# Performance work log

Hardware: AMD Instinct MI355X
Metric: run time of the kernel (lower is better)

## Reference

```python
import jax, jax.numpy as jnp
import numpy as np

B, H = 1024, 256
HP = H // 2  # hyperparams_dim
W_SCALE = 0.08  # kaiming-uniform-like magnitude to keep tanh unsaturated


def setup_inputs() -> dict:
    key = jax.random.key(0)
    ks = jax.random.split(key, 8)
    return {
        "h_0": jax.random.normal(ks[0], (B, 1, H), dtype=jnp.float32),
        "h_t": jax.random.normal(ks[1], (B, 1, H), dtype=jnp.float32),
        "msg": jax.random.normal(ks[2], (B, 1, H), dtype=jnp.float32),
        "c": jax.random.uniform(ks[3], (1,), dtype=jnp.float32),
        "fc1_w": jax.random.normal(ks[4], (HP, H), dtype=jnp.float32) * W_SCALE,
        "fc2_w": jax.random.normal(ks[5], (HP, HP), dtype=jnp.float32) * W_SCALE,
        "fc3_w": jax.random.normal(ks[6], (HP, HP), dtype=jnp.float32) * W_SCALE,
        "fc4_w": jax.random.normal(ks[7], (2 * H * H, HP), dtype=jnp.float32) * W_SCALE,
    }


def reference(h_0, h_t, msg, c, fc1_w, fc2_w, fc3_w, fc4_w):
    # torch code clamps self.c into [0, 1] before use
    cc = jnp.clip(c, 0.0, 1.0)
    h = cc * h_0 + (1.0 - cc) * h_t                     # [B, 1, H]
    x = jnp.tanh(jnp.einsum('bsh,ph->bsp', h, fc1_w))    # [B, 1, HP]
    x = jnp.tanh(jnp.einsum('bsp,qp->bsq', x, fc2_w))    # [B, 1, HP]
    x = jnp.tanh(jnp.einsum('bsq,rq->bsr', x, fc3_w))    # [B, 1, HP]
    f4 = jnp.einsum('bsr,wr->bsw', x, fc4_w)             # [B, 1, 2*H*H]
    g1 = f4[..., : H * H].reshape(-1, H, H)              # [B, H, H]
    g2 = f4[..., H * H :].reshape(-1, H, H)              # [B, H, H]
    # F.linear(msg[i], g) == msg[i] @ g.T, batched over B
    g1_out = jnp.tanh(jnp.einsum('bsh,bkh->bsk', msg, g1))  # [B, 1, H]
    out = jnp.einsum('bsk,bok->bso', g1_out, g2)             # [B, 1, H]
    return out
```

## Files before the change

### kernel.cpp

```cpp
#include <hip/hip_runtime.h>
#include <hip/hip_bf16.h>

#define HDIM 256
#define HPDIM 128

typedef short bf8 __attribute__((ext_vector_type(8)));
typedef float f32x4 __attribute__((ext_vector_type(4)));

__device__ inline unsigned pkbf2(float a, float b) {
  float2 f; f.x = a; f.y = b;
  __hip_bfloat162 h = __float22bfloat162_rn(f);
  unsigned u; __builtin_memcpy(&u, &h, 4); return u;
}
__device__ inline unsigned short bfbits(float v) {
  __hip_bfloat16 h = __float2bfloat16(v);
  unsigned short u; __builtin_memcpy(&u, &h, 2); return u;
}
__device__ inline uint4 pack8u(float4 a, float4 b) {
  uint4 r;
  r.x = pkbf2(a.x, a.y); r.y = pkbf2(a.z, a.w);
  r.z = pkbf2(b.x, b.y); r.w = pkbf2(b.z, b.w);
  return r;
}
__device__ inline float fast_tanh(float x) {
  float t = __expf(2.0f * x);
  return 1.0f - 2.0f * __builtin_amdgcn_rcpf(t + 1.0f);
}

__global__ __launch_bounds__(256) void k_fmt(
    const float* __restrict__ w1, const float* __restrict__ w2,
    const float* __restrict__ w3, const float* __restrict__ msg,
    short* __restrict__ wf, float* __restrict__ msgTT) {
  __shared__ float T[64][257];
  const int t = threadIdx.x;
  if (blockIdx.x < 32) {
    int u = blockIdx.x * 256 + t;
    const float* src; short* dst; int row, c, Kt;
    if (u < 4096)      { src = w1; dst = wf;          Kt = 8; row = u >> 5; c = u & 31; }
    else if (u < 6144) { src = w2; dst = wf + 32768;  Kt = 4; row = (u-4096) >> 4; c = (u-4096) & 15; }
    else               { src = w3; dst = wf + 49152;  Kt = 4; row = (u-6144) >> 4; c = (u-6144) & 15; }
    int ks = c >> 2, q = c & 3, Kd = Kt * 32;
    const float* s = src + row * Kd + ks * 32 + q * 8;
    float4 a = *(const float4*)s, b = *(const float4*)(s + 4);
    int P = row >> 4, r16 = row & 15;
    int outl = ((P * Kt + ks) * 64 + q * 16 + r16);
    *(uint4*)(dst + (size_t)outl * 8) = pack8u(a, b);
  } else {
    const int b0 = (blockIdx.x - 32) * 64;
    #pragma unroll 4
    for (int it = 0; it < 16; ++it) {
      int flat = it * 1024 + t * 4;
      int row = flat >> 8, col = flat & 255;
      float4 v = *(const float4*)(msg + (b0 + row) * HDIM + col);
      T[row][col] = v.x; T[row][col+1] = v.y; T[row][col+2] = v.z; T[row][col+3] = v.w;
    }
    __syncthreads();
    const int bloc = t & 63;
    #pragma unroll 4
    for (int it = 0; it < 16; ++it) {
      int g = it * 4 + (t >> 6);
      float4 v; v.x = T[bloc][g*4]; v.y = T[bloc][g*4+1];
                v.z = T[bloc][g*4+2]; v.w = T[bloc][g*4+3];
      *(float4*)(msgTT + (size_t)g * 4096 + (b0 + bloc) * 4) = v;
    }
  }
}

__global__ __launch_bounds__(256) void k_mlp(
    const float* __restrict__ h0, const float* __restrict__ htv,
    const float* __restrict__ cp, const short* __restrict__ wf,
    short* __restrict__ x3f) {
  __shared__ char hbuf[8192];
  __shared__ char xa[4096];
  __shared__ char xb[4096];
  const int t = threadIdx.x, wave = t >> 6, lane = t & 63;
  const int r16 = lane & 15, quad = lane >> 4;
  const int b0 = blockIdx.x * 16;
  const float cc = fminf(fmaxf(cp[0], 0.f), 1.f);

  #pragma unroll
  for (int it = 0; it < 2; ++it) {
    int flat = it * 2048 + t * 8;
    int row = flat >> 8, col = flat & 255, kb = col >> 3;
    int gi = (b0 + row) * HDIM + col;
    float4 a = *(const float4*)(h0 + gi);
    float4 b = *(const float4*)(htv + gi);
    float4 va, vb;
    va.x = cc*a.x + (1.f-cc)*b.x; va.y = cc*a.y + (1.f-cc)*b.y;
    va.z = cc*a.z + (1.f-cc)*b.z; va.w = cc*a.w + (1.f-cc)*b.w;
    a = *(const float4*)(h0 + gi + 4); b = *(const float4*)(htv + gi + 4);
    vb.x = cc*a.x + (1.f-cc)*b.x; vb.y = cc*a.y + (1.f-cc)*b.y;
    vb.z = cc*a.z + (1.f-cc)*b.z; vb.w = cc*a.w + (1.f-cc)*b.w;
    *(uint4*)(hbuf + row*512 + ((kb ^ (row & 7)) << 4)) = pack8u(va, vb);
  }
  __syncthreads();

  {
    f32x4 acc[2] = {};
    #pragma unroll
    for (int ks = 0; ks < 8; ++ks) {
      bf8 af = *(bf8*)(hbuf + r16*512 + (((ks*4 + quad) ^ (r16 & 7)) << 4));
      #pragma unroll
      for (int nt = 0; nt < 2; ++nt) {
        bf8 bw_ = *(const bf8*)(wf + (size_t)(((wave*2 + nt)*8 + ks)*64 + lane)*8);
        acc[nt] = __builtin_amdgcn_mfma_f32_16x16x32_bf16(af, bw_, acc[nt], 0, 0, 0);
      }
    }
    #pragma unroll
    for (int nt = 0; nt < 2; ++nt)
      #pragma unroll
      for (int i = 0; i < 4; ++i) {
        int row = quad*4 + i, col = wave*32 + nt*16 + r16;
        *(unsigned short*)(xa + row*256 + (((col >> 3) ^ (row & 7)) << 4) + ((col & 7) << 1))
            = bfbits(fast_tanh(acc[nt][i]));
      }
  }
  __syncthreads();
  {
    f32x4 acc[2] = {};
    #pragma unroll
    for (int ks = 0; ks < 4; ++ks) {
      bf8 af = *(bf8*)(xa + r16*256 + (((ks*4 + quad) ^ (r16 & 7)) << 4));
      #pragma unroll
      for (int nt = 0; nt < 2; ++nt) {
        bf8 bw_ = *(const bf8*)(wf + 32768 + (size_t)(((wave*2 + nt)*4 + ks)*64 + lane)*8);
        acc[nt] = __builtin_amdgcn_mfma_f32_16x16x32_bf16(af, bw_, acc[nt], 0, 0, 0);
      }
    }
    #pragma unroll
    for (int nt = 0; nt < 2; ++nt)
      #pragma unroll
      for (int i = 0; i < 4; ++i) {
        int row = quad*4 + i, col = wave*32 + nt*16 + r16;
        *(unsigned short*)(xb + row*256 + (((col >> 3) ^ (row & 7)) << 4) + ((col & 7) << 1))
            = bfbits(fast_tanh(acc[nt][i]));
      }
  }
  __syncthreads();
  {
    f32x4 acc[2] = {};
    #pragma unroll
    for (int ks = 0; ks < 4; ++ks) {
      bf8 af = *(bf8*)(xb + r16*256 + (((ks*4 + quad) ^ (r16 & 7)) << 4));
      #pragma unroll
      for (int nt = 0; nt < 2; ++nt) {
        bf8 bw_ = *(const bf8*)(wf + 49152 + (size_t)(((wave*2 + nt)*4 + ks)*64 + lane)*8);
        acc[nt] = __builtin_amdgcn_mfma_f32_16x16x32_bf16(af, bw_, acc[nt], 0, 0, 0);
      }
    }
    #pragma unroll
    for (int nt = 0; nt < 2; ++nt)
      #pragma unroll
      for (int i = 0; i < 4; ++i) {
        int row = quad*4 + i, col = wave*32 + nt*16 + r16;
        *(unsigned short*)(xa + row*256 + (((col >> 3) ^ (row & 7)) << 4) + ((col & 7) << 1))
            = bfbits(fast_tanh(acc[nt][i]));
      }
  }
  __syncthreads();
  {
    int ks = t >> 6, l = t & 63, q2 = l >> 4, rr = l & 15;
    uint4 d = *(uint4*)(xa + rr*256 + (((ks*4 + q2) ^ (rr & 7)) << 4));
    *(uint4*)(x3f + (size_t)((blockIdx.x*4 + ks)*64 + l)*8) = d;
  }
}

template<int PHASE>
__global__ __launch_bounds__(256, 4) void k_hyper(
    const short* __restrict__ x3f, const float* __restrict__ wTT,
    const float* __restrict__ fc4, float* __restrict__ outp) {
  __shared__ char lds[32768];
  const int kcol = blockIdx.x;
  const int t = threadIdx.x, wave = t >> 6, lane = t & 63;
  const int r16 = lane & 15, quad = lane >> 4;
  const int bw = blockIdx.y * 256 + wave * 64;

  bf8 xf[4][4];
  #pragma unroll
  for (int nt = 0; nt < 4; ++nt)
    #pragma unroll
    for (int ks = 0; ks < 4; ++ks)
      xf[nt][ks] = *(const bf8*)(x3f +
          (size_t)(((blockIdx.y*16 + wave*4 + nt)*4 + ks)*64 + lane)*8);

  const float* src = fc4 + ((size_t)(PHASE ? 65536 : 0) + (size_t)kcol * 256) * HPDIM;
  float gacc[4] = {0.f, 0.f, 0.f, 0.f};

  #pragma unroll 1
  for (int half = 0; half < 2; ++half) {
    #pragma unroll
    for (int it = 0; it < 8; ++it) {
      int flat = it * 2048 + t * 8;
      int row = flat >> 7, kb = t & 15;
      float4 a = *(const float4*)(src + half*16384 + flat);
      float4 b = *(const float4*)(src + half*16384 + flat + 4);
      *(uint4*)(lds + row*256 + ((kb ^ (row & 7)) << 4)) = pack8u(a, b);
    }
    __syncthreads();

    #pragma unroll 2
    for (int ht = 0; ht < 8; ++ht) {
      const int hb = half*32 + ht*4 + quad;
      float4 wv[4];
      #pragma unroll
      for (int nt = 0; nt < 4; ++nt)
        wv[nt] = *(const float4*)(wTT + (size_t)hb*4096 + (bw + nt*16 + r16)*4);
      const int row = ht*16 + r16;
      bf8 af[4];
      #pragma unroll
      for (int ks = 0; ks < 4; ++ks)
        af[ks] = *(bf8*)(lds + row*256 + (((ks*4 + quad) ^ (row & 7)) << 4));
      #pragma unroll
      for (int nt = 0; nt < 4; ++nt) {
        f32x4 acc = {};
        #pragma unroll
        for (int ks = 0; ks < 4; ++ks)
          acc = __builtin_amdgcn_mfma_f32_16x16x32_bf16(af[ks], xf[nt][ks], acc, 0, 0, 0);
        gacc[nt] += acc[0]*wv[nt].x + acc[1]*wv[nt].y + acc[2]*wv[nt].z + acc[3]*wv[nt].w;
      }
    }
    __syncthreads();
  }

  #pragma unroll
  for (int nt = 0; nt < 4; ++nt) {
    float v = gacc[nt];
    v += __shfl_xor(v, 16);
    v += __shfl_xor(v, 32);
    if (quad == 0) {
      int b = bw + nt*16 + r16;
      if (PHASE == 0) outp[(size_t)(kcol >> 2)*4096 + b*4 + (kcol & 3)] = fast_tanh(v);
      else            outp[b*HDIM + kcol] = v;
    }
  }
}

extern "C" void kernel_launch(void* const* d_in, const int* in_sizes, int n_in,
                              void* d_out, int out_size, void* d_ws, size_t ws_size,
                              hipStream_t stream) {
  const float* h0  = (const float*)d_in[0];
  const float* htt = (const float*)d_in[1];
  const float* msg = (const float*)d_in[2];
  const float* c   = (const float*)d_in[3];
  const float* w1  = (const float*)d_in[4];
  const float* w2  = (const float*)d_in[5];
  const float* w3  = (const float*)d_in[6];
  const float* w4  = (const float*)d_in[7];
  float* out = (float*)d_out;

  short* x3f  = (short*)d_ws;
  float* g1TT = (float*)((char*)d_ws + 262144);
  float* msgTT= (float*)((char*)d_ws + 262144 + 1048576);
  short* wf   = (short*)((char*)d_ws + 262144 + 2097152);

  k_fmt<<<dim3(48), dim3(256), 0, stream>>>(w1, w2, w3, msg, wf, msgTT);
  k_mlp<<<dim3(64), dim3(256), 0, stream>>>(h0, htt, c, wf, x3f);
  k_hyper<0><<<dim3(256, 4), dim3(256), 0, stream>>>(x3f, msgTT, w4, g1TT);
  k_hyper<1><<<dim3(256, 4), dim3(256), 0, stream>>>(x3f, g1TT, w4, out);
}
```

Measured before the change: 182.5 us.

## Pre-convert fc4 to bf16 once, stream it with async LDS loads, merge prep kernels

A new prep kernel converts the whole fc4 weight to swizzled bf16 in workspace, transposes msg, and runs the MLP, which now reads fp32 w1-w3 directly. This merges three small launches into one. The hyper kernels then load the bf16 tiles with global_load_lds in double-buffered quarters, which halves the fc4 bytes each hyper block reads and overlaps loads with MFMA. Block indices are swizzled for L2 locality and occupancy is lowered to 3 blocks per SM. The cost is an extra full fc4 read plus a bf16 write inside the timed prep kernel.

```diff
diff --git a/kernel.cpp b/kernel.cpp
--- a/kernel.cpp
+++ b/kernel.cpp
@@ -26,56 +26,62 @@
   float t = __expf(2.0f * x);
   return 1.0f - 2.0f * __builtin_amdgcn_rcpf(t + 1.0f);
 }
-
-__global__ __launch_bounds__(256) void k_fmt(
+__device__ inline bf8 wfrag(const float* __restrict__ s) {
+  float4 a = *(const float4*)s, b = *(const float4*)(s + 4);
+  uint4 u = pack8u(a, b);
+  bf8 r; __builtin_memcpy(&r, &u, 16); return r;
+}
+
+typedef const __attribute__((address_space(1))) unsigned int* gas_ptr;
+typedef __attribute__((address_space(3))) unsigned int* las_ptr;
+__device__ inline void gld_lds16(const void* g, void* l) {
+  __builtin_amdgcn_global_load_lds((gas_ptr)g, (las_ptr)l, 16, 0, 0);
+}
+
+__global__ __launch_bounds__(256) void k_prep(
+    const float* __restrict__ h0, const float* __restrict__ htv,
+    const float* __restrict__ cp,
     const float* __restrict__ w1, const float* __restrict__ w2,
     const float* __restrict__ w3, const float* __restrict__ msg,
-    short* __restrict__ wf, float* __restrict__ msgTT) {
-  __shared__ float T[64][257];
+    const float* __restrict__ fc4,
+    short* __restrict__ x3f, float* __restrict__ msgTT,
+    short* __restrict__ fc4f) {
   const int t = threadIdx.x;
-  if (blockIdx.x < 32) {
-    int u = blockIdx.x * 256 + t;
-    const float* src; short* dst; int row, c, Kt;
-    if (u < 4096)      { src = w1; dst = wf;          Kt = 8; row = u >> 5; c = u & 31; }
-    else if (u < 6144) { src = w2; dst = wf + 32768;  Kt = 4; row = (u-4096) >> 4; c = (u-4096) & 15; }
-    else               { src = w3; dst = wf + 49152;  Kt = 4; row = (u-6144) >> 4; c = (u-6144) & 15; }
-    int ks = c >> 2, q = c & 3, Kd = Kt * 32;
-    const float* s = src + row * Kd + ks * 32 + q * 8;
-    float4 a = *(const float4*)s, b = *(const float4*)(s + 4);
-    int P = row >> 4, r16 = row & 15;
-    int outl = ((P * Kt + ks) * 64 + q * 16 + r16);
-    *(uint4*)(dst + (size_t)outl * 8) = pack8u(a, b);
-  } else {
-    const int b0 = (blockIdx.x - 32) * 64;
-    #pragma unroll 4
+  const int bx = blockIdx.x;
+
+  if (bx >= 80) {
+    const int tile = bx - 80;
+    const float* srcp = fc4 + (size_t)tile * (64 * 128);
+    char* dstp = (char*)fc4f + (size_t)tile * (64 * 256);
+    #pragma unroll
+    for (int it = 0; it < 4; ++it) {
+      int cid = it * 256 + t;
+      int rl = cid >> 4, c = cid & 15;
+      const float* s = srcp + rl * 128 + c * 8;
+      float4 a = *(const float4*)s, b = *(const float4*)(s + 4);
+      *(uint4*)(dstp + rl * 256 + ((c ^ (rl & 7)) << 4)) = pack8u(a, b);
+    }
+    return;
+  }
+
+  if (bx >= 64) {
+    const int b0 = (bx - 64) * 64;
+    #pragma unroll
     for (int it = 0; it < 16; ++it) {
-      int flat = it * 1024 + t * 4;
-      int row = flat >> 8, col = flat & 255;
-      float4 v = *(const float4*)(msg + (b0 + row) * HDIM + col);
-      T[row][col] = v.x; T[row][col+1] = v.y; T[row][col+2] = v.z; T[row][col+3] = v.w;
-    }
-    __syncthreads();
-    const int bloc = t & 63;
-    #pragma unroll 4
-    for (int it = 0; it < 16; ++it) {
-      int g = it * 4 + (t >> 6);
-      float4 v; v.x = T[bloc][g*4]; v.y = T[bloc][g*4+1];
-                v.z = T[bloc][g*4+2]; v.w = T[bloc][g*4+3];
-      *(float4*)(msgTT + (size_t)g * 4096 + (b0 + bloc) * 4) = v;
-    }
-  }
-}
-
-__global__ __launch_bounds__(256) void k_mlp(
-    const float* __restrict__ h0, const float* __restrict__ htv,
-    const float* __restrict__ cp, const short* __restrict__ wf,
-    short* __restrict__ x3f) {
+      int u = it * 256 + t;
+      int bl = u & 63, g = u >> 6;
+      float4 v = *(const float4*)(msg + (size_t)(b0 + bl) * HDIM + g * 4);
+      *(float4*)(msgTT + (size_t)g * 4096 + (b0 + bl) * 4) = v;
+    }
+    return;
+  }
+
   __shared__ char hbuf[8192];
   __shared__ char xa[4096];
   __shared__ char xb[4096];
-  const int t = threadIdx.x, wave = t >> 6, lane = t & 63;
+  const int wave = t >> 6, lane = t & 63;
   const int r16 = lane & 15, quad = lane >> 4;
-  const int b0 = blockIdx.x * 16;
+  const int b0 = bx * 16;
   const float cc = fminf(fmaxf(cp[0], 0.f), 1.f);
 
   #pragma unroll
@@ -102,7 +108,7 @@
       bf8 af = *(bf8*)(hbuf + r16*512 + (((ks*4 + quad) ^ (r16 & 7)) << 4));
       #pragma unroll
       for (int nt = 0; nt < 2; ++nt) {
-        bf8 bw_ = *(const bf8*)(wf + (size_t)(((wave*2 + nt)*8 + ks)*64 + lane)*8);
+        bf8 bw_ = wfrag(w1 + ((wave*2 + nt)*16 + r16) * 256 + ks*32 + quad*8);
         acc[nt] = __builtin_amdgcn_mfma_f32_16x16x32_bf16(af, bw_, acc[nt], 0, 0, 0);
       }
     }
@@ -123,7 +129,7 @@
       bf8 af = *(bf8*)(xa + r16*256 + (((ks*4 + quad) ^ (r16 & 7)) << 4));
       #pragma unroll
       for (int nt = 0; nt < 2; ++nt) {
-        bf8 bw_ = *(const bf8*)(wf + 32768 + (size_t)(((wave*2 + nt)*4 + ks)*64 + lane)*8);
+        bf8 bw_ = wfrag(w2 + ((wave*2 + nt)*16 + r16) * 128 + ks*32 + quad*8);
         acc[nt] = __builtin_amdgcn_mfma_f32_16x16x32_bf16(af, bw_, acc[nt], 0, 0, 0);
       }
     }
@@ -144,7 +150,7 @@
       bf8 af = *(bf8*)(xb + r16*256 + (((ks*4 + quad) ^ (r16 & 7)) << 4));
       #pragma unroll
       for (int nt = 0; nt < 2; ++nt) {
-        bf8 bw_ = *(const bf8*)(wf + 49152 + (size_t)(((wave*2 + nt)*4 + ks)*64 + lane)*8);
+        bf8 bw_ = wfrag(w3 + ((wave*2 + nt)*16 + r16) * 128 + ks*32 + quad*8);
         acc[nt] = __builtin_amdgcn_mfma_f32_16x16x32_bf16(af, bw_, acc[nt], 0, 0, 0);
       }
     }
@@ -161,16 +167,17 @@
   {
     int ks = t >> 6, l = t & 63, q2 = l >> 4, rr = l & 15;
     uint4 d = *(uint4*)(xa + rr*256 + (((ks*4 + q2) ^ (rr & 7)) << 4));
-    *(uint4*)(x3f + (size_t)((blockIdx.x*4 + ks)*64 + l)*8) = d;
+    *(uint4*)(x3f + (size_t)((bx*4 + ks)*64 + l)*8) = d;
   }
 }
 
 template<int PHASE>
-__global__ __launch_bounds__(256, 4) void k_hyper(
+__global__ __launch_bounds__(256, 3) void k_hyper(
     const short* __restrict__ x3f, const float* __restrict__ wTT,
-    const float* __restrict__ fc4, float* __restrict__ outp) {
-  __shared__ char lds[32768];
-  const int kcol = blockIdx.x;
+    const short* __restrict__ fc4f, float* __restrict__ outp) {
+  __shared__ char lds[2 * 16384];
+  const int bxs = blockIdx.x;
+  const int kcol = ((bxs & 7) << 5) | (bxs >> 3);
   const int t = threadIdx.x, wave = t >> 6, lane = t & 63;
   const int r16 = lane & 15, quad = lane >> 4;
   const int bw = blockIdx.y * 256 + wave * 64;
@@ -183,33 +190,43 @@
       xf[nt][ks] = *(const bf8*)(x3f +
           (size_t)(((blockIdx.y*16 + wave*4 + nt)*4 + ks)*64 + lane)*8);
 
-  const float* src = fc4 + ((size_t)(PHASE ? 65536 : 0) + (size_t)kcol * 256) * HPDIM;
+  const char* src = (const char*)fc4f +
+      ((size_t)(PHASE ? 65536 : 0) + (size_t)kcol * 256) * 256;
+
+  #pragma unroll
+  for (int it = 0; it < 4; ++it)
+    gld_lds16(src + it*4096 + t*16, (char*)lds + it*4096 + t*16);
+  __syncthreads();
+
   float gacc[4] = {0.f, 0.f, 0.f, 0.f};
+  const float* wbase = wTT + (size_t)quad * 4096 + (bw + r16) * 4;
 
   #pragma unroll 1
-  for (int half = 0; half < 2; ++half) {
-    #pragma unroll
-    for (int it = 0; it < 8; ++it) {
-      int flat = it * 2048 + t * 8;
-      int row = flat >> 7, kb = t & 15;
-      float4 a = *(const float4*)(src + half*16384 + flat);
-      float4 b = *(const float4*)(src + half*16384 + flat + 4);
-      *(uint4*)(lds + row*256 + ((kb ^ (row & 7)) << 4)) = pack8u(a, b);
-    }
-    __syncthreads();
-
-    #pragma unroll 2
-    for (int ht = 0; ht < 8; ++ht) {
-      const int hb = half*32 + ht*4 + quad;
-      float4 wv[4];
-      #pragma unroll
-      for (int nt = 0; nt < 4; ++nt)
-        wv[nt] = *(const float4*)(wTT + (size_t)hb*4096 + (bw + nt*16 + r16)*4);
-      const int row = ht*16 + r16;
+  for (int q = 0; q < 4; ++q) {
+    char* buf = (char*)lds + (q & 1) * 16384;
+    float4 wv[4];
+    #pragma unroll
+    for (int nt = 0; nt < 4; ++nt)
+      wv[nt] = *(const float4*)(wbase + (size_t)(q * 16) * 4096 + nt * 64);
+    if (q < 3) {
+      char* nbuf = (char*)lds + ((q + 1) & 1) * 16384;
+      const char* nsrc = src + (q + 1) * 16384;
+      #pragma unroll
+      for (int it = 0; it < 4; ++it)
+        gld_lds16(nsrc + it*4096 + t*16, nbuf + it*4096 + t*16);
+    }
+    #pragma unroll
+    for (int htl = 0; htl < 4; ++htl) {
+      if (htl > 0) {
+        #pragma unroll
+        for (int nt = 0; nt < 4; ++nt)
+          wv[nt] = *(const float4*)(wbase + (size_t)(q*16 + htl*4) * 4096 + nt * 64);
+      }
+      const int row = htl * 16 + r16;
       bf8 af[4];
       #pragma unroll
       for (int ks = 0; ks < 4; ++ks)
-        af[ks] = *(bf8*)(lds + row*256 + (((ks*4 + quad) ^ (row & 7)) << 4));
+        af[ks] = *(bf8*)(buf + row*256 + (((ks*4 + quad) ^ (row & 7)) << 4));
       #pragma unroll
       for (int nt = 0; nt < 4; ++nt) {
         f32x4 acc = {};
@@ -251,10 +268,10 @@
   short* x3f  = (short*)d_ws;
   float* g1TT = (float*)((char*)d_ws + 262144);
   float* msgTT= (float*)((char*)d_ws + 262144 + 1048576);
-  short* wf   = (short*)((char*)d_ws + 262144 + 2097152);
-
-  k_fmt<<<dim3(48), dim3(256), 0, stream>>>(w1, w2, w3, msg, wf, msgTT);
-  k_mlp<<<dim3(64), dim3(256), 0, stream>>>(h0, htt, c, wf, x3f);
-  k_hyper<0><<<dim3(256, 4), dim3(256), 0, stream>>>(x3f, msgTT, w4, g1TT);
-  k_hyper<1><<<dim3(256, 4), dim3(256), 0, stream>>>(x3f, g1TT, w4, out);
-}
+  short* fc4f = (short*)((char*)d_ws + 262144 + 2097152);
+
+  k_prep<<<dim3(2128), dim3(256), 0, stream>>>(h0, htt, c, w1, w2, w3, msg, w4,
+                                               x3f, msgTT, fc4f);
+  k_hyper<0><<<dim3(256, 4), dim3(256), 0, stream>>>(x3f, msgTT, fc4f, g1TT);
+  k_hyper<1><<<dim3(256, 4), dim3(256), 0, stream>>>(x3f, g1TT, fc4f, out);
+}
```

Result: faster. 178.6 us (-2.1%).
